# Optimization experiments

Hardware: AMD Instinct MI355X
Metric: run time of the kernel (lower is better)

## Reference

```python
import jax, jax.numpy as jnp
import numpy as np

DT = 0.025    # ms, integration time step
CM = 1.0      # uF/cm^2 membrane capacitance
E_NA, E_K, E_L = 50.0, -77.0, -54.387  # mV reversal potentials

T, N = 8192, 2048


def setup_inputs() -> dict:
    key = jax.random.key(0)
    ks = jax.random.split(key, 5)
    return {
        "input_estim": 5.0 * jax.random.normal(ks[0], (T, N), dtype=jnp.float32),  # uA/cm^2 stim per segment per step
        "V0": -65.0 + 2.0 * jax.random.normal(ks[1], (N,), dtype=jnp.float32),
        "m0": 0.05 + 0.02 * jax.random.uniform(ks[2], (N,), dtype=jnp.float32),
        "h0": 0.60 + 0.05 * jax.random.uniform(ks[3], (N,), dtype=jnp.float32),
        "n0": 0.32 + 0.05 * jax.random.uniform(ks[4], (N,), dtype=jnp.float32),
        "g_na": 120.0 * jnp.ones((N,), jnp.float32),
        "g_k": 36.0 * jnp.ones((N,), jnp.float32),
        "g_l": 0.3 * jnp.ones((N,), jnp.float32),
        "g_ax": 5.0 * jnp.ones((N,), jnp.float32),  # axial coupling conductance between neighbor segments
    }


def _rates(V):
    am = 0.1 * (V + 40.0) / (1.0 - jnp.exp(-(V + 40.0) / 10.0))
    bm = 4.0 * jnp.exp(-(V + 65.0) / 18.0)
    ah = 0.07 * jnp.exp(-(V + 65.0) / 20.0)
    bh = 1.0 / (1.0 + jnp.exp(-(V + 35.0) / 10.0))
    an = 0.01 * (V + 55.0) / (1.0 - jnp.exp(-(V + 55.0) / 10.0))
    bn = 0.125 * jnp.exp(-(V + 65.0) / 80.0)
    return am, bm, ah, bh, an, bn


def reference(input_estim, V0, m0, h0, n0, g_na, g_k, g_l, g_ax):
    def step(state, i_stim):
        V, m, h, n = state
        am, bm, ah, bh, an, bn = _rates(V)
        i_ion = (g_na * m**3 * h * (V - E_NA)
                 + g_k * n**4 * (V - E_K)
                 + g_l * (V - E_L))
        # sealed-end cable: zero-flux boundaries via edge padding
        Vp = jnp.pad(V, (1, 1), mode="edge")
        i_ax = g_ax * (Vp[:-2] + Vp[2:] - 2.0 * V)
        dV = (i_ax + i_stim - i_ion) / CM
        # total transmembrane current (capacitive + ionic) = axial + stim
        mem_cur = CM * dV + i_ion
        new_state = (V + DT * dV,
                     m + DT * (am * (1.0 - m) - bm * m),
                     h + DT * (ah * (1.0 - h) - bh * h),
                     n + DT * (an * (1.0 - n) - bn * n))
        return new_state, (mem_cur, V)

    state0 = (V0, m0, h0, n0)
    (Vf, mf, hf, nf), (mem_currents, mem_voltages) = jax.lax.scan(step, state0, input_estim)
    # (mem_currents_over_time, mem_voltage_over_time, final state)
    return mem_currents, mem_voltages, Vf, mf, hf, nf
```

## Files before the change

### kernel.cpp

```cpp
#include <hip/hip_runtime.h>

typedef unsigned long long u64;
typedef unsigned int u32;

#define TSTEPS 8192
#define NSEG   2048
#define DTC    0.025f

#define KST    28
#define KTAIL  16
#define WAVE   64
#define COWN   8
#define NBLK   (NSEG / COWN)
#define NPH    ((TSTEPS + KST - 1) / KST)
#define JLO    KST

constexpr double L2E = 1.4426950408889634074;

#define AM_A ((float)(-0.1 * L2E))
#define CEM  0.018315638888734179f
#define CEH  0.030197383422318501f
#define CEN  0.0040867714384640666f
#define BM_A ((float)(-L2E / 18.0))
#define BM_B ((float)(2.0 - 65.0 * L2E / 18.0))
#define QA   ((float)(-L2E / 80.0))
#define QB   ((float)(-65.0 * L2E / 80.0))
#define CAH  0.2645751311064591f

#define AL(p) __hip_atomic_load((p), __ATOMIC_RELAXED, __HIP_MEMORY_SCOPE_AGENT)
#define AS(p, v) __hip_atomic_store((p), (v), __ATOMIC_RELAXED, __HIP_MEMORY_SCOPE_AGENT)

__device__ __forceinline__ u64 pack_tag(float v, int tag) {
    return ((u64)(u32)tag << 32) | (u64)__float_as_uint(v);
}
__device__ __forceinline__ float lo_f(u64 w) { return __uint_as_float((u32)w); }
__device__ __forceinline__ float bperm(int addr, float v) {
    return __int_as_float(__builtin_amdgcn_ds_bpermute(addr, __float_as_int(v)));
}

template <int KS, int KN>
__device__ __forceinline__ void run_phase(
    int p, int b, int j, int s, int sc,
    bool owned, int addrL, int addrR,
    float gna, float gk, float gl, float gax,
    const float* __restrict__ stim, u64* __restrict__ tstate,
    float* __restrict__ out_cur, float* __restrict__ out_volt,
    float2* lbuf, float (&st)[KST],
    float& V, float& m, float& h, float& n, bool pub)
{
    const int t0 = p * KST;

    const bool needLoad = (!owned) || (p == 0);
    const u64* sb = tstate + (size_t)(p & 1) * 4 * NSEG + sc;
    {
        u64 w0 = 0, w1 = 0, w2 = 0, w3 = 0;
        int ok;
        do {
            ok = 1;
            if (needLoad) {
                w0 = AL(sb);            w1 = AL(sb + NSEG);
                w2 = AL(sb + 2 * NSEG); w3 = AL(sb + 3 * NSEG);
                ok = (int)(w0 >> 32) >= p && (int)(w1 >> 32) >= p &&
                     (int)(w2 >> 32) >= p && (int)(w3 >> 32) >= p;
            }
        } while (!__all(ok));
        if (needLoad) {
            V = lo_f(w0); m = lo_f(w1); h = lo_f(w2); n = lo_f(w3);
        }
    }

    float Vl = bperm(addrL, V);
    float Vr = bperm(addrR, V);

    const int jo = j - JLO;
#pragma unroll
    for (int k = 0; k < KS; ++k) {
        const float is = st[k];
        const float ax = (Vl + Vr) - 2.0f * V;
        const float mc = __builtin_fmaf(gax, ax, is);
        const float m3 = m * m * m;
        const float n2 = n * n;
        const float i_ion = gna * m3 * h * (V - 50.0f)
                          + gk * (n2 * n2) * (V + 77.0f)
                          + gl * (V + 54.387f);
        const float dV = mc - i_ion;
        const float Vn = __builtin_fmaf(DTC, dV, V);
        const float VlN = bperm(addrL, Vn);
        const float VrN = bperm(addrR, Vn);

        if (owned) lbuf[k * COWN + jo] = make_float2(mc, V);

        const float em0 = __builtin_amdgcn_exp2f(V * AM_A);
        const float am  = __builtin_fmaf(0.1f, V, 4.0f) *
                          __builtin_amdgcn_rcpf(__builtin_fmaf(-CEM, em0, 1.0f));
        const float an  = __builtin_fmaf(0.01f, V, 0.55f) *
                          __builtin_amdgcn_rcpf(__builtin_fmaf(-CEN, em0, 1.0f));
        const float bh  = __builtin_amdgcn_rcpf(__builtin_fmaf(CEH, em0, 1.0f));
        const float bm  = __builtin_amdgcn_exp2f(__builtin_fmaf(V, BM_A, BM_B));
        const float q   = __builtin_amdgcn_exp2f(__builtin_fmaf(V, QA, QB));
        const float tq  = CAH * (q * q);
        const float ah  = tq * tq;
        const float bn  = 0.125f * q;

        m = __builtin_fmaf(DTC, __builtin_fmaf(-(am + bm), m, am), m);
        h = __builtin_fmaf(DTC, __builtin_fmaf(-(ah + bh), h, ah), h);
        n = __builtin_fmaf(DTC, __builtin_fmaf(-(an + bn), n, an), n);
        V = Vn; Vl = VlN; Vr = VrN;
    }

    if (pub && owned) {
        u64* pb = tstate + (size_t)((p + 1) & 1) * 4 * NSEG + s;
        AS(pb,            pack_tag(V, p + 1));
        AS(pb + NSEG,     pack_tag(m, p + 1));
        AS(pb + 2 * NSEG, pack_tag(h, p + 1));
        AS(pb + 3 * NSEG, pack_tag(n, p + 1));
    }
    __builtin_amdgcn_sched_barrier(0);

    if (KN > 0) {
        const float* spn = stim + (size_t)(t0 + KST) * NSEG + sc;
#pragma unroll
        for (int u = 0; u < KN; ++u)
            st[u] = spn[(size_t)u * NSEG];
    }
    __builtin_amdgcn_sched_barrier(0);

    const int sbase = b * COWN;
#pragma unroll
    for (int base = 0; base < KS * COWN; base += WAVE) {
        const int idx = base + j;
        if (idx < KS * COWN) {
            const float2 v = lbuf[idx];
            const size_t go = (size_t)(t0 + (idx >> 3)) * NSEG + sbase + (idx & 7);
            __builtin_nontemporal_store(v.x, out_cur + go);
            __builtin_nontemporal_store(v.y, out_volt + go);
        }
    }
}

__global__ __launch_bounds__(WAVE, 1) void hh_persist(
    const float* __restrict__ stim,
    const float* __restrict__ gna_p, const float* __restrict__ gk_p,
    const float* __restrict__ gl_p,  const float* __restrict__ gax_p,
    u64* __restrict__ tstate,
    float* __restrict__ out_cur, float* __restrict__ out_volt,
    float* __restrict__ tail)
{
    const int j = threadIdx.x;
    const int b = blockIdx.x;
    const int s = b * COWN - KST + j;
    const int sc = s < 0 ? 0 : (s > NSEG - 1 ? NSEG - 1 : s);
    const bool owned = (j >= JLO) && (j < JLO + COWN);

    const int jl = (s <= 0)        ? j : (j > 0  ? j - 1 : 0);
    const int jr = (s >= NSEG - 1) ? j : (j < 63 ? j + 1 : 63);
    const int addrL = jl * 4;
    const int addrR = jr * 4;

    const float gna = gna_p[sc], gk = gk_p[sc], gl = gl_p[sc], gax = gax_p[sc];

    __shared__ float2 lbuf[KST * COWN];

    float V = 0.f, m = 0.f, h = 0.f, n = 0.f;
    float st[KST];

#pragma unroll
    for (int u = 0; u < KST; ++u)
        st[u] = stim[(size_t)u * NSEG + sc];
    __builtin_amdgcn_sched_barrier(0);

    for (int p = 0; p < NPH - 2; ++p)
        run_phase<KST, KST>(p, b, j, s, sc, owned, addrL, addrR,
                            gna, gk, gl, gax, stim, tstate,
                            out_cur, out_volt, lbuf, st, V, m, h, n, true);
    run_phase<KST, KTAIL>(NPH - 2, b, j, s, sc, owned, addrL, addrR,
                          gna, gk, gl, gax, stim, tstate,
                          out_cur, out_volt, lbuf, st, V, m, h, n, true);
    run_phase<KTAIL, 0>(NPH - 1, b, j, s, sc, owned, addrL, addrR,
                        gna, gk, gl, gax, stim, tstate,
                        out_cur, out_volt, lbuf, st, V, m, h, n, false);

    if (owned) {
        tail[s] = V; tail[NSEG + s] = m;
        tail[2 * NSEG + s] = h; tail[3 * NSEG + s] = n;
    }
}

__global__ void hh_init(const float* __restrict__ V0, const float* __restrict__ m0,
                        const float* __restrict__ h0, const float* __restrict__ n0,
                        u64* __restrict__ tstate)
{
    const int i = blockIdx.x * blockDim.x + threadIdx.x;
    if (i < NSEG) {
        tstate[i]            = pack_tag(V0[i], 0);
        tstate[NSEG + i]     = pack_tag(m0[i], 0);
        tstate[2 * NSEG + i] = pack_tag(h0[i], 0);
        tstate[3 * NSEG + i] = pack_tag(n0[i], 0);
        u64* b1 = tstate + 4 * NSEG;
        const u64 inv = (u64)(u32)0x80000000u << 32;
        b1[i] = inv; b1[NSEG + i] = inv; b1[2 * NSEG + i] = inv; b1[3 * NSEG + i] = inv;
    }
}

extern "C" void kernel_launch(void* const* d_in, const int* in_sizes, int n_in,
                              void* d_out, int out_size, void* d_ws, size_t ws_size,
                              hipStream_t stream)
{
    const float* stim = (const float*)d_in[0];
    const float* V0   = (const float*)d_in[1];
    const float* m0   = (const float*)d_in[2];
    const float* h0   = (const float*)d_in[3];
    const float* n0   = (const float*)d_in[4];
    const float* gna  = (const float*)d_in[5];
    const float* gk   = (const float*)d_in[6];
    const float* gl   = (const float*)d_in[7];
    const float* gax  = (const float*)d_in[8];

    float* out      = (float*)d_out;
    float* out_cur  = out;
    float* out_volt = out + (size_t)TSTEPS * NSEG;
    float* tail     = out + 2 * (size_t)TSTEPS * NSEG;

    u64* tstate = (u64*)d_ws;

    hipLaunchKernelGGL(hh_init, dim3(8), dim3(256), 0, stream,
                       V0, m0, h0, n0, tstate);
    hipLaunchKernelGGL(hh_persist, dim3(NBLK), dim3(WAVE), 0, stream,
                       stim, gna, gk, gl, gax, tstate,
                       out_cur, out_volt, tail);
}
```

Before: 1.194 ms.

## Double-buffer stimulus prefetch and shorten per-step dependency chain

The next phase's stimulus loads now go into a second register array and are issued before the current phase's compute loop, so their latency is hidden behind the time steps instead of sitting on the critical path after publishing. The ionic current is refactored into a conductance-times-V plus constant form so the V update depends on fewer serial operations. The three reciprocals in the rate functions are merged into one rcp with extra multiplies. Together these double stimulus register usage (pressure on a 64-thread wave) and change rounding slightly.

```diff
diff --git a/kernel.cpp b/kernel.cpp
--- a/kernel.cpp
+++ b/kernel.cpp
@@ -42,10 +42,10 @@
 __device__ __forceinline__ void run_phase(
     int p, int b, int j, int s, int sc,
     bool owned, int addrL, int addrR,
-    float gna, float gk, float gl, float gax,
+    float gna, float gk, float gl, float gax, float Kgl,
     const float* __restrict__ stim, u64* __restrict__ tstate,
     float* __restrict__ out_cur, float* __restrict__ out_volt,
-    float2* lbuf, float (&st)[KST],
+    float2* lbuf, float (&stC)[KST], float (&stN)[KST],
     float& V, float& m, float& h, float& n, bool pub)
 {
     const int t0 = p * KST;
@@ -69,21 +69,33 @@
         }
     }
 
+    if (KN > 0) {
+        const float* spn = stim + (size_t)(t0 + KST) * NSEG + sc;
+#pragma unroll
+        for (int u = 0; u < KN; ++u)
+            stN[u] = spn[(size_t)u * NSEG];
+    }
+    __builtin_amdgcn_sched_barrier(0);
+
     float Vl = bperm(addrL, V);
     float Vr = bperm(addrR, V);
 
     const int jo = j - JLO;
 #pragma unroll
     for (int k = 0; k < KS; ++k) {
-        const float is = st[k];
-        const float ax = (Vl + Vr) - 2.0f * V;
-        const float mc = __builtin_fmaf(gax, ax, is);
         const float m3 = m * m * m;
+        const float P1 = gna * m3 * h;
         const float n2 = n * n;
-        const float i_ion = gna * m3 * h * (V - 50.0f)
-                          + gk * (n2 * n2) * (V + 77.0f)
-                          + gl * (V + 54.387f);
-        const float dV = mc - i_ion;
+        const float P2 = gk * (n2 * n2);
+        const float G  = (P1 + P2) + gl;
+        const float C  = __builtin_fmaf(77.0f, P2,
+                          __builtin_fmaf(-50.0f, P1, Kgl));
+
+        const float t  = Vl + Vr;
+        const float ax = __builtin_fmaf(-2.0f, V, t);
+        const float mc = __builtin_fmaf(gax, ax, stC[k]);
+        const float ii = __builtin_fmaf(G, V, C);
+        const float dV = mc - ii;
         const float Vn = __builtin_fmaf(DTC, dV, V);
         const float VlN = bperm(addrL, Vn);
         const float VrN = bperm(addrR, Vn);
@@ -91,11 +103,15 @@
         if (owned) lbuf[k * COWN + jo] = make_float2(mc, V);
 
         const float em0 = __builtin_amdgcn_exp2f(V * AM_A);
-        const float am  = __builtin_fmaf(0.1f, V, 4.0f) *
-                          __builtin_amdgcn_rcpf(__builtin_fmaf(-CEM, em0, 1.0f));
-        const float an  = __builtin_fmaf(0.01f, V, 0.55f) *
-                          __builtin_amdgcn_rcpf(__builtin_fmaf(-CEN, em0, 1.0f));
-        const float bh  = __builtin_amdgcn_rcpf(__builtin_fmaf(CEH, em0, 1.0f));
+        const float da  = __builtin_fmaf(-CEM, em0, 1.0f);
+        const float db  = __builtin_fmaf(-CEN, em0, 1.0f);
+        const float dc  = __builtin_fmaf( CEH, em0, 1.0f);
+        const float dab = da * db;
+        const float r3  = __builtin_amdgcn_rcpf(dab * dc);
+        const float rab = dc * r3;
+        const float am  = __builtin_fmaf(0.1f, V, 4.0f)   * (db * rab);
+        const float an  = __builtin_fmaf(0.01f, V, 0.55f) * (da * rab);
+        const float bh  = dab * r3;
         const float bm  = __builtin_amdgcn_exp2f(__builtin_fmaf(V, BM_A, BM_B));
         const float q   = __builtin_amdgcn_exp2f(__builtin_fmaf(V, QA, QB));
         const float tq  = CAH * (q * q);
@@ -114,14 +130,6 @@
         AS(pb + NSEG,     pack_tag(m, p + 1));
         AS(pb + 2 * NSEG, pack_tag(h, p + 1));
         AS(pb + 3 * NSEG, pack_tag(n, p + 1));
-    }
-    __builtin_amdgcn_sched_barrier(0);
-
-    if (KN > 0) {
-        const float* spn = stim + (size_t)(t0 + KST) * NSEG + sc;
-#pragma unroll
-        for (int u = 0; u < KN; ++u)
-            st[u] = spn[(size_t)u * NSEG];
     }
     __builtin_amdgcn_sched_barrier(0);
 
@@ -158,27 +166,35 @@
     const int addrR = jr * 4;
 
     const float gna = gna_p[sc], gk = gk_p[sc], gl = gl_p[sc], gax = gax_p[sc];
+    const float Kgl = 54.387f * gl;
 
     __shared__ float2 lbuf[KST * COWN];
 
     float V = 0.f, m = 0.f, h = 0.f, n = 0.f;
-    float st[KST];
+    float stA[KST], stB[KST];
 
 #pragma unroll
     for (int u = 0; u < KST; ++u)
-        st[u] = stim[(size_t)u * NSEG + sc];
+        stA[u] = stim[(size_t)u * NSEG + sc];
     __builtin_amdgcn_sched_barrier(0);
 
-    for (int p = 0; p < NPH - 2; ++p)
-        run_phase<KST, KST>(p, b, j, s, sc, owned, addrL, addrR,
-                            gna, gk, gl, gax, stim, tstate,
-                            out_cur, out_volt, lbuf, st, V, m, h, n, true);
-    run_phase<KST, KTAIL>(NPH - 2, b, j, s, sc, owned, addrL, addrR,
-                          gna, gk, gl, gax, stim, tstate,
-                          out_cur, out_volt, lbuf, st, V, m, h, n, true);
-    run_phase<KTAIL, 0>(NPH - 1, b, j, s, sc, owned, addrL, addrR,
-                        gna, gk, gl, gax, stim, tstate,
-                        out_cur, out_volt, lbuf, st, V, m, h, n, false);
+    for (int p = 0; p < 290; p += 2) {
+        run_phase<KST, KST>(p,     b, j, s, sc, owned, addrL, addrR,
+                            gna, gk, gl, gax, Kgl, stim, tstate,
+                            out_cur, out_volt, lbuf, stA, stB, V, m, h, n, true);
+        run_phase<KST, KST>(p + 1, b, j, s, sc, owned, addrL, addrR,
+                            gna, gk, gl, gax, Kgl, stim, tstate,
+                            out_cur, out_volt, lbuf, stB, stA, V, m, h, n, true);
+    }
+    run_phase<KST, KST>(290, b, j, s, sc, owned, addrL, addrR,
+                        gna, gk, gl, gax, Kgl, stim, tstate,
+                        out_cur, out_volt, lbuf, stA, stB, V, m, h, n, true);
+    run_phase<KST, KTAIL>(291, b, j, s, sc, owned, addrL, addrR,
+                          gna, gk, gl, gax, Kgl, stim, tstate,
+                          out_cur, out_volt, lbuf, stB, stA, V, m, h, n, true);
+    run_phase<KTAIL, 0>(292, b, j, s, sc, owned, addrL, addrR,
+                        gna, gk, gl, gax, Kgl, stim, tstate,
+                        out_cur, out_volt, lbuf, stA, stB, V, m, h, n, false);
 
     if (owned) {
         tail[s] = V; tail[NSEG + s] = m;
```

New measurement: 1.320 ms. +10.5%, slower.

## Double-buffer LDS output and stimulus registers to overlap stores with compute

Applied to the files above, without the earlier changes.

The LDS staging buffer and the stimulus register array are now double-buffered. Each phase writes out the previous phase's outputs and prefetches the next phase's stimulus right after the neighbor-state poll, before the compute loop. Previously this happened after publishing the state. The aim is to take the store issue and load latency off the critical path between publish and the next phase's wait. In exchange it doubles register use for stimulus (28 to 56 floats) and doubles LDS, and the phase loop is unrolled by two with hardcoded phase counts.

```diff
diff --git a/kernel.cpp b/kernel.cpp
--- a/kernel.cpp
+++ b/kernel.cpp
@@ -38,14 +38,14 @@
     return __int_as_float(__builtin_amdgcn_ds_bpermute(addr, __float_as_int(v)));
 }
 
-template <int KS, int KN>
+template <int KS, int KN, int KP>
 __device__ __forceinline__ void run_phase(
     int p, int b, int j, int s, int sc,
     bool owned, int addrL, int addrR,
     float gna, float gk, float gl, float gax,
     const float* __restrict__ stim, u64* __restrict__ tstate,
     float* __restrict__ out_cur, float* __restrict__ out_volt,
-    float2* lbuf, float (&st)[KST],
+    float2* cur, float2* prv, float (&stC)[KST], float (&stN)[KST],
     float& V, float& m, float& h, float& n, bool pub)
 {
     const int t0 = p * KST;
@@ -68,14 +68,37 @@
             V = lo_f(w0); m = lo_f(w1); h = lo_f(w2); n = lo_f(w3);
         }
     }
+    __builtin_amdgcn_sched_barrier(0);
+
+    if (KP > 0) {
+        const int t0p = t0 - KST;
+        const int sbase = b * COWN;
+#pragma unroll
+        for (int base = 0; base < KP * COWN; base += WAVE) {
+            const int idx = base + j;
+            if (idx < KP * COWN) {
+                const float2 v = prv[idx];
+                const size_t go = (size_t)(t0p + (idx >> 3)) * NSEG + sbase + (idx & 7);
+                __builtin_nontemporal_store(v.x, out_cur + go);
+                __builtin_nontemporal_store(v.y, out_volt + go);
+            }
+        }
+    }
+
+    if (KN > 0) {
+        const float* spn = stim + (size_t)(t0 + KST) * NSEG + sc;
+#pragma unroll
+        for (int u = 0; u < KN; ++u)
+            stN[u] = spn[(size_t)u * NSEG];
+    }
+    __builtin_amdgcn_sched_barrier(0);
 
     float Vl = bperm(addrL, V);
     float Vr = bperm(addrR, V);
-
     const int jo = j - JLO;
 #pragma unroll
     for (int k = 0; k < KS; ++k) {
-        const float is = st[k];
+        const float is = stC[k];
         const float ax = (Vl + Vr) - 2.0f * V;
         const float mc = __builtin_fmaf(gax, ax, is);
         const float m3 = m * m * m;
@@ -88,7 +111,7 @@
         const float VlN = bperm(addrL, Vn);
         const float VrN = bperm(addrR, Vn);
 
-        if (owned) lbuf[k * COWN + jo] = make_float2(mc, V);
+        if (owned) cur[k * COWN + jo] = make_float2(mc, V);
 
         const float em0 = __builtin_amdgcn_exp2f(V * AM_A);
         const float am  = __builtin_fmaf(0.1f, V, 4.0f) *
@@ -115,27 +138,6 @@
         AS(pb + 2 * NSEG, pack_tag(h, p + 1));
         AS(pb + 3 * NSEG, pack_tag(n, p + 1));
     }
-    __builtin_amdgcn_sched_barrier(0);
-
-    if (KN > 0) {
-        const float* spn = stim + (size_t)(t0 + KST) * NSEG + sc;
-#pragma unroll
-        for (int u = 0; u < KN; ++u)
-            st[u] = spn[(size_t)u * NSEG];
-    }
-    __builtin_amdgcn_sched_barrier(0);
-
-    const int sbase = b * COWN;
-#pragma unroll
-    for (int base = 0; base < KS * COWN; base += WAVE) {
-        const int idx = base + j;
-        if (idx < KS * COWN) {
-            const float2 v = lbuf[idx];
-            const size_t go = (size_t)(t0 + (idx >> 3)) * NSEG + sbase + (idx & 7);
-            __builtin_nontemporal_store(v.x, out_cur + go);
-            __builtin_nontemporal_store(v.y, out_volt + go);
-        }
-    }
 }
 
 __global__ __launch_bounds__(WAVE, 1) void hh_persist(
@@ -159,27 +161,48 @@
 
     const float gna = gna_p[sc], gk = gk_p[sc], gl = gl_p[sc], gax = gax_p[sc];
 
-    __shared__ float2 lbuf[KST * COWN];
+    __shared__ float2 pl0[KST * COWN], pl1[KST * COWN];
 
     float V = 0.f, m = 0.f, h = 0.f, n = 0.f;
-    float st[KST];
+    float stA[KST], stB[KST];
 
 #pragma unroll
     for (int u = 0; u < KST; ++u)
-        st[u] = stim[(size_t)u * NSEG + sc];
+        stA[u] = stim[(size_t)u * NSEG + sc];
     __builtin_amdgcn_sched_barrier(0);
 
-    for (int p = 0; p < NPH - 2; ++p)
-        run_phase<KST, KST>(p, b, j, s, sc, owned, addrL, addrR,
-                            gna, gk, gl, gax, stim, tstate,
-                            out_cur, out_volt, lbuf, st, V, m, h, n, true);
-    run_phase<KST, KTAIL>(NPH - 2, b, j, s, sc, owned, addrL, addrR,
-                          gna, gk, gl, gax, stim, tstate,
-                          out_cur, out_volt, lbuf, st, V, m, h, n, true);
-    run_phase<KTAIL, 0>(NPH - 1, b, j, s, sc, owned, addrL, addrR,
-                        gna, gk, gl, gax, stim, tstate,
-                        out_cur, out_volt, lbuf, st, V, m, h, n, false);
-
+    run_phase<KST, KST, 0>(0, b, j, s, sc, owned, addrL, addrR,
+                           gna, gk, gl, gax, stim, tstate, out_cur, out_volt,
+                           pl0, pl1, stA, stB, V, m, h, n, true);
+    for (int p = 1; p < 291; p += 2) {
+        run_phase<KST, KST, KST>(p,     b, j, s, sc, owned, addrL, addrR,
+                                 gna, gk, gl, gax, stim, tstate, out_cur, out_volt,
+                                 pl1, pl0, stB, stA, V, m, h, n, true);
+        run_phase<KST, KST, KST>(p + 1, b, j, s, sc, owned, addrL, addrR,
+                                 gna, gk, gl, gax, stim, tstate, out_cur, out_volt,
+                                 pl0, pl1, stA, stB, V, m, h, n, true);
+    }
+    run_phase<KST, KTAIL, KST>(291, b, j, s, sc, owned, addrL, addrR,
+                               gna, gk, gl, gax, stim, tstate, out_cur, out_volt,
+                               pl1, pl0, stB, stA, V, m, h, n, true);
+    run_phase<KTAIL, 0, KST>(292, b, j, s, sc, owned, addrL, addrR,
+                             gna, gk, gl, gax, stim, tstate, out_cur, out_volt,
+                             pl0, pl1, stA, stB, V, m, h, n, false);
+
+    {
+        const int t0 = 292 * KST;
+        const int sbase = b * COWN;
+#pragma unroll
+        for (int base = 0; base < KTAIL * COWN; base += WAVE) {
+            const int idx = base + j;
+            if (idx < KTAIL * COWN) {
+                const float2 v = pl0[idx];
+                const size_t go = (size_t)(t0 + (idx >> 3)) * NSEG + sbase + (idx & 7);
+                __builtin_nontemporal_store(v.x, out_cur + go);
+                __builtin_nontemporal_store(v.y, out_volt + go);
+            }
+        }
+    }
     if (owned) {
         tail[s] = V; tail[NSEG + s] = m;
         tail[2 * NSEG + s] = h; tail[3 * NSEG + s] = n;
```

After: 1.364 ms. 14.2% more time.
